# Kernel optimization log

Measured on AMD Instinct MI355X. Metric: run time of the kernel, lower is better.

Reference implementation:

```python
import jax, jax.numpy as jnp
import numpy as np

L = 8          # num_layers
D = 1024       # embed_size
H = 16         # num_heads
M = 4096       # mlp_size
V = 64         # token_size
TMAX = 2048    # max_tokens
B, T = 4, 2048
EPS = 1e-5


def setup_inputs() -> dict:
    key = jax.random.key(0)
    ks = jax.random.split(key, 16)
    s = 0.02
    return {
        "toks": jax.random.normal(ks[0], (B, T, V), dtype=jnp.float32),
        "W_tok": jax.random.normal(ks[1], (D, V), dtype=jnp.float32) * s,    # token_embedding.weight [out,in]
        "W_pos": jax.random.normal(ks[2], (D, TMAX), dtype=jnp.float32) * s,  # postn_embedding.weight
        "Wqkv": jax.random.normal(ks[3], (L, 3 * D, D), dtype=jnp.float32) * s,
        "g1": jnp.ones((L, D), dtype=jnp.float32),
        "be1": jnp.zeros((L, D), dtype=jnp.float32),
        "W1": jax.random.normal(ks[4], (L, M, D), dtype=jnp.float32) * s,
        "bm1": jnp.zeros((L, M), dtype=jnp.float32),
        "W2": jax.random.normal(ks[5], (L, D, M), dtype=jnp.float32) * s,
        "bm2": jnp.zeros((L, D), dtype=jnp.float32),
        "g2": jnp.ones((L, D), dtype=jnp.float32),
        "be2": jnp.zeros((L, D), dtype=jnp.float32),
        "gf": jnp.ones((D,), dtype=jnp.float32),
        "bf": jnp.zeros((D,), dtype=jnp.float32),
        "Wun": jax.random.normal(ks[6], (V, D), dtype=jnp.float32) * s,
        "bun": jnp.zeros((V,), dtype=jnp.float32),
    }


def _layernorm(x, g, b):
    mu = jnp.mean(x, axis=-1, keepdims=True)
    var = jnp.mean(jnp.square(x - mu), axis=-1, keepdims=True)
    return (x - mu) * jax.lax.rsqrt(var + EPS) * g + b


def _attention(x, Wqkv, mask):
    Bx, Tx, Dx = x.shape
    c = Dx // H
    # matches torch: view(B,T,H,3c) then split -> Q/K/V interleaved per head
    qkv = (x @ Wqkv.T).reshape(Bx, Tx, H, 3 * c).transpose(0, 2, 1, 3)  # [B,H,T,3c]
    q, k, v = jnp.split(qkv, 3, axis=-1)
    A = jnp.einsum("bhtc,bhsc->bhts", q, k) / (c ** 0.5)
    A = A + mask  # additive log-mask (0 / -inf), as in the torch code
    p = jax.nn.softmax(A, axis=-1)
    y = jnp.einsum("bhts,bhsc->bhtc", p, v)
    return y.transpose(0, 2, 1, 3).reshape(Bx, Tx, Dx)


def reference(toks, W_tok, W_pos, Wqkv, g1, be1, W1, bm1, W2, bm2, g2, be2, gf, bf, Wun, bun):
    Bx, Tx, _ = toks.shape
    mask = jnp.where(jnp.tril(jnp.ones((Tx, Tx), dtype=bool)), 0.0, -jnp.inf).astype(toks.dtype)
    x = toks @ W_tok.T + W_pos.T[:Tx, :]
    for l in range(L):
        # NOTE: DTransformer adds an EXTRA residual around each block: x = x + block(x)
        h = x
        h = h + _attention(_layernorm(h, g1[l], be1[l]), Wqkv[l], mask)
        z = _layernorm(h, g2[l], be2[l])
        h = h + (jax.nn.relu(z @ W1[l].T + bm1[l]) @ W2[l].T + bm2[l])
        x = x + h
    return _layernorm(x, gf, bf) @ Wun.T + bun
```

## Files before the change

### kernel.cpp

```cpp
#include <hip/hip_runtime.h>
#include <cstdint>
#include <cstddef>

#define L_NUM 8
#define D_DIM 1024
#define H_NUM 16
#define C_DIM 64
#define M_DIM 4096
#define V_DIM 64
#define B_SZ 4
#define T_SZ 2048
#define N_TOK (B_SZ * T_SZ)
#define TMAXP 2048
#define QKV_LD (3 * D_DIM)

typedef __bf16 bf16;
typedef bf16 bf16x4 __attribute__((ext_vector_type(4)));
typedef bf16 bf16x8 __attribute__((ext_vector_type(8)));
typedef float f32x4v __attribute__((ext_vector_type(4)));

__device__ __forceinline__ void async16(const bf16* g, bf16* l) {
    __builtin_amdgcn_global_load_lds(
        (const __attribute__((address_space(1))) void*)g,
        (__attribute__((address_space(3))) void*)l, 16, 0, 0);
}

__global__ __launch_bounds__(256) void convert_kernel(const float* __restrict__ src,
                                                      bf16* __restrict__ dst, int n) {
    int i = (blockIdx.x * 256 + threadIdx.x) * 4;
    if (i >= n) return;
    const float4 v = *(const float4*)(src + i);
    bf16x4 o;
    o[0] = (bf16)v.x; o[1] = (bf16)v.y; o[2] = (bf16)v.z; o[3] = (bf16)v.w;
    *(bf16x4*)(dst + i) = o;
}

__global__ __launch_bounds__(256) void transpose_pos(const float* __restrict__ in,
                                                     float* __restrict__ out) {
    __shared__ float tile[32][33];
    const int t0 = blockIdx.x * 32, d0 = blockIdx.y * 32;
    const int tx = threadIdx.x & 31, ty = threadIdx.x >> 5;
#pragma unroll
    for (int j = 0; j < 32; j += 8)
        tile[ty + j][tx] = in[(size_t)(d0 + ty + j) * TMAXP + t0 + tx];
    __syncthreads();
#pragma unroll
    for (int j = 0; j < 32; j += 8)
        out[(size_t)(t0 + ty + j) * D_DIM + d0 + tx] = tile[tx][ty + j];
}

__global__ __launch_bounds__(256) void ln_kernel(const float* __restrict__ x,
                                                 const float* __restrict__ g,
                                                 const float* __restrict__ b,
                                                 bf16* __restrict__ y) {
    const int n = blockIdx.x, tid = threadIdx.x;
    const float4 v = ((const float4*)(x + (size_t)n * D_DIM))[tid];
    float s = v.x + v.y + v.z + v.w;
    float q = v.x * v.x + v.y * v.y + v.z * v.z + v.w * v.w;
#pragma unroll
    for (int off = 32; off > 0; off >>= 1) {
        s += __shfl_xor(s, off);
        q += __shfl_xor(q, off);
    }
    __shared__ float s1[4], s2[4];
    if ((tid & 63) == 0) { s1[tid >> 6] = s; s2[tid >> 6] = q; }
    __syncthreads();
    s = s1[0] + s1[1] + s1[2] + s1[3];
    q = s2[0] + s2[1] + s2[2] + s2[3];
    const float mu = s * (1.f / D_DIM);
    const float var = q * (1.f / D_DIM) - mu * mu;
    const float rs = rsqrtf(var + 1e-5f);
    const float4 gg = ((const float4*)g)[tid];
    const float4 bb = ((const float4*)b)[tid];
    bf16x4 o;
    o[0] = (bf16)((v.x - mu) * rs * gg.x + bb.x);
    o[1] = (bf16)((v.y - mu) * rs * gg.y + bb.y);
    o[2] = (bf16)((v.z - mu) * rs * gg.z + bb.z);
    o[3] = (bf16)((v.w - mu) * rs * gg.w + bb.w);
    ((bf16x4*)(y + (size_t)n * D_DIM))[tid] = o;
}

template <int MODE>
__global__ __launch_bounds__(256) void gemm_bt(const bf16* __restrict__ A,
                                               const bf16* __restrict__ W,
                                               const float* __restrict__ bias,
                                               const float* add1, const float* add2,
                                               float* outF, bf16* outB, int K, int Nc) {
    __shared__ __align__(16) bf16 As[128][64];
    __shared__ __align__(16) bf16 Bs[128][64];
    const int tid = threadIdx.x;
    const int lane = tid & 63, w = tid >> 6;
    const int wm = w >> 1, wn = w & 1;
    const int l15 = lane & 15, quad = lane >> 4;
    const size_t rowbase = (size_t)blockIdx.y * 128;
    const size_t colbase = (size_t)blockIdx.x * 128;
    f32x4v acc[4][4] = {};
    const int rsub = lane >> 3;
    const int schunk = lane & 7;
    const int gchunk = schunk ^ rsub;
    const bf16* Ag = A + (rowbase + w * 32 + rsub) * (size_t)K + gchunk * 8;
    const bf16* Wg = W + (colbase + w * 32 + rsub) * (size_t)K + gchunk * 8;
    bf16* Asl = &As[w * 32][0];
    bf16* Bsl = &Bs[w * 32][0];
    const int swz = l15 & 7;
    for (int k0 = 0; k0 < K; k0 += 64) {
        __syncthreads();
#pragma unroll
        for (int i = 0; i < 4; ++i) {
            async16(Ag + k0 + (size_t)(i * 8) * K, Asl + i * 512);
            async16(Wg + k0 + (size_t)(i * 8) * K, Bsl + i * 512);
        }
        __syncthreads();
#pragma unroll
        for (int kk = 0; kk < 2; ++kk) {
            const int q = kk * 4 + quad;
            bf16x8 af[4], bv[4];
#pragma unroll
            for (int f = 0; f < 4; ++f) {
                af[f] = *(const bf16x8*)&As[wm * 64 + f * 16 + l15][(q ^ swz) * 8];
                bv[f] = *(const bf16x8*)&Bs[wn * 64 + f * 16 + l15][(q ^ swz) * 8];
            }
#pragma unroll
            for (int fm = 0; fm < 4; ++fm)
#pragma unroll
                for (int fn = 0; fn < 4; ++fn)
                    acc[fm][fn] = __builtin_amdgcn_mfma_f32_16x16x32_bf16(af[fm], bv[fn], acc[fm][fn], 0, 0, 0);
        }
    }
    float bcol[4];
    if (MODE == 1 || MODE == 2) {
#pragma unroll
        for (int fn = 0; fn < 4; ++fn) bcol[fn] = bias[colbase + wn * 64 + fn * 16 + l15];
    }
#pragma unroll
    for (int fm = 0; fm < 4; ++fm) {
#pragma unroll
        for (int r = 0; r < 4; ++r) {
            const size_t row = rowbase + wm * 64 + fm * 16 + quad * 4 + r;
            const size_t base = row * (size_t)Nc + colbase + wn * 64 + l15;
#pragma unroll
            for (int fn = 0; fn < 4; ++fn) {
                float v = acc[fm][fn][r];
                const size_t idx = base + fn * 16;
                if (MODE == 0) {
                    outB[idx] = (bf16)v;
                } else if (MODE == 1) {
                    v += bcol[fn];
                    outB[idx] = (bf16)fmaxf(v, 0.f);
                } else if (MODE == 2) {
                    v += bcol[fn] + add1[idx] + add2[idx];
                    outF[idx] = v;
                } else {
                    const size_t t = row & (T_SZ - 1);
                    const size_t col = colbase + wn * 64 + fn * 16 + l15;
                    v += add1[t * (size_t)Nc + col];
                    outF[idx] = v;
                }
            }
        }
    }
}

template <int MODE>
__global__ __launch_bounds__(512, 2) void gemm256_bt(const bf16* __restrict__ A,
                                                     const bf16* __restrict__ W,
                                                     const float* __restrict__ bias,
                                                     float* outF, bf16* outB, int K, int Nc) {
    __shared__ __align__(16) bf16 As[2][256][64];
    __shared__ __align__(16) bf16 Bs[2][256][64];
    const int tid = threadIdx.x;
    const int lane = tid & 63, w = tid >> 6;
    const int wm = w >> 2, wn = w & 3;
    const int l15 = lane & 15, quad = lane >> 4;
    const size_t rowbase = (size_t)blockIdx.y * 256;
    const size_t colbase = (size_t)blockIdx.x * 256;
    f32x4v acc[8][4] = {};
    const int rsub = lane >> 3;
    const int schunk = lane & 7;
    const int gchunk = schunk ^ rsub;
    const bf16* Ag = A + (rowbase + w * 32 + rsub) * (size_t)K + gchunk * 8;
    const bf16* Wg = W + (colbase + w * 32 + rsub) * (size_t)K + gchunk * 8;
    const int swz = l15 & 7;
    const int nk = K / 64;
#pragma unroll
    for (int i = 0; i < 4; ++i) {
        async16(Ag + (size_t)(i * 8) * K, &As[0][w * 32][0] + i * 512);
        async16(Wg + (size_t)(i * 8) * K, &Bs[0][w * 32][0] + i * 512);
    }
    __syncthreads();
    for (int t = 0; t < nk; ++t) {
        const int cur = t & 1;
        if (t + 1 < nk) {
            const size_t ko = (size_t)(t + 1) * 64;
#pragma unroll
            for (int i = 0; i < 4; ++i) {
                async16(Ag + ko + (size_t)(i * 8) * K, &As[cur ^ 1][w * 32][0] + i * 512);
                async16(Wg + ko + (size_t)(i * 8) * K, &Bs[cur ^ 1][w * 32][0] + i * 512);
            }
        }
        __builtin_amdgcn_s_setprio(1);
#pragma unroll
        for (int kk = 0; kk < 2; ++kk) {
            const int q = kk * 4 + quad;
            bf16x8 af[8], bv[4];
#pragma unroll
            for (int f = 0; f < 8; ++f)
                af[f] = *(const bf16x8*)&As[cur][wm * 128 + f * 16 + l15][(q ^ swz) * 8];
#pragma unroll
            for (int f = 0; f < 4; ++f)
                bv[f] = *(const bf16x8*)&Bs[cur][wn * 64 + f * 16 + l15][(q ^ swz) * 8];
#pragma unroll
            for (int fm = 0; fm < 8; ++fm)
#pragma unroll
                for (int fn = 0; fn < 4; ++fn)
                    acc[fm][fn] = __builtin_amdgcn_mfma_f32_16x16x32_bf16(af[fm], bv[fn], acc[fm][fn], 0, 0, 0);
        }
        __builtin_amdgcn_s_setprio(0);
        __syncthreads();
    }
    float bcol[4];
    if (MODE == 1) {
#pragma unroll
        for (int fn = 0; fn < 4; ++fn) bcol[fn] = bias[colbase + wn * 64 + fn * 16 + l15];
    }
#pragma unroll
    for (int fm = 0; fm < 8; ++fm) {
#pragma unroll
        for (int r = 0; r < 4; ++r) {
            const size_t row = rowbase + wm * 128 + fm * 16 + quad * 4 + r;
            const size_t base = row * (size_t)Nc + colbase + wn * 64 + l15;
#pragma unroll
            for (int fn = 0; fn < 4; ++fn) {
                float v = acc[fm][fn][r];
                const size_t idx = base + fn * 16;
                if (MODE == 1) {
                    v += bcol[fn];
                    outB[idx] = (bf16)fmaxf(v, 0.f);
                } else {
                    outF[idx] = v;
                }
            }
        }
    }
}

__global__ __launch_bounds__(256) void attn_kernel(const bf16* __restrict__ qkv,
                                                   const float* __restrict__ x,
                                                   float* __restrict__ h) {
    constexpr int NQT = T_SZ / 128;
    const int pair = blockIdx.x;
    const int hh = blockIdx.y, b = blockIdx.z;
    const int tid = threadIdx.x;
    const int lane = tid & 63, w = tid >> 6;
    const int quad = lane >> 4, l15 = lane & 15;

    __shared__ __align__(16) bf16 Ks[64][64];
    __shared__ __align__(16) bf16 Vt[64][72];
    __shared__ __align__(16) bf16 Ps[4][16][80];

    constexpr float SC = 0.125f * 1.44269504f;

    const int krow = lane >> 3;
    const int kchunk = lane & 7;
    const int kswz = kchunk ^ krow;
    const bf16* kbase = qkv + ((size_t)(b * T_SZ) + w * 16 + krow) * QKV_LD +
                        hh * 192 + 64 + kchunk * 8;
    const bf16* vbase0 = qkv + ((size_t)(b * T_SZ) + w * 8) * QKV_LD + hh * 192 + 128 + lane;
    const bf16* vbase1 = qkv + ((size_t)(b * T_SZ) + (w + 4) * 8) * QKV_LD + hh * 192 + 128 + lane;

    for (int half = 0; half < 2; ++half) {
        const int qt = half ? (NQT - 1 - pair) : pair;
        const int qwave = qt * 128 + w * 32;
        const int nst = 2 * qt + 2;

        bf16x8 Qf[2][2];
#pragma unroll
        for (int qsub = 0; qsub < 2; ++qsub)
#pragma unroll
            for (int kc = 0; kc < 2; ++kc)
                Qf[qsub][kc] = *(const bf16x8*)(qkv +
                    ((size_t)(b * T_SZ + qt * 128 + w * 32 + qsub * 16 + l15)) * QKV_LD +
                    hh * 192 + kc * 32 + quad * 8);

        f32x4v accO[2][4] = {};
        float m_[2] = {-1e30f, -1e30f}, l_[2] = {0.f, 0.f};

        const bf16* kptr = kbase;
        const bf16* vptr0 = vbase0;
        const bf16* vptr1 = vbase1;

        uint4 kr0 = *(const uint4*)(kptr);
        uint4 kr1 = *(const uint4*)(kptr + (size_t)8 * QKV_LD);
        bf16x8 vv0, vv1;
#pragma unroll
        for (int j = 0; j < 8; ++j) { vv0[j] = vptr0[(size_t)j * QKV_LD]; vv1[j] = vptr1[(size_t)j * QKV_LD]; }
        kptr += (size_t)64 * QKV_LD; vptr0 += (size_t)64 * QKV_LD; vptr1 += (size_t)64 * QKV_LD;

        for (int st = 0; st < nst; ++st) {
            const int sbase = st * 64;
            __syncthreads();
            *(uint4*)&Ks[w * 16 + krow][kswz * 8] = kr0;
            *(uint4*)&Ks[w * 16 + 8 + krow][kswz * 8] = kr1;
            *(bf16x8*)&Vt[lane][w * 8] = vv0;
            *(bf16x8*)&Vt[lane][(w + 4) * 8] = vv1;
            __syncthreads();
            if (st + 1 < nst) {
                kr0 = *(const uint4*)(kptr);
                kr1 = *(const uint4*)(kptr + (size_t)8 * QKV_LD);
#pragma unroll
                for (int j = 0; j < 8; ++j) { vv0[j] = vptr0[(size_t)j * QKV_LD]; vv1[j] = vptr1[(size_t)j * QKV_LD]; }
                kptr += (size_t)64 * QKV_LD; vptr0 += (size_t)64 * QKV_LD; vptr1 += (size_t)64 * QKV_LD;
            }
            if (sbase <= qwave + 31) {
#pragma unroll
                for (int qsub = 0; qsub < 2; ++qsub) {
                    const int qb = qwave + qsub * 16;
                    f32x4v St[4] = {};
                    __builtin_amdgcn_s_setprio(1);
#pragma unroll
                    for (int ssub = 0; ssub < 4; ++ssub)
#pragma unroll
                        for (int kc = 0; kc < 2; ++kc) {
                            bf16x8 Kf = *(const bf16x8*)&Ks[ssub * 16 + l15][((kc * 4 + quad) ^ (l15 & 7)) * 8];
                            St[ssub] = __builtin_amdgcn_mfma_f32_16x16x32_bf16(Kf, Qf[qsub][kc], St[ssub], 0, 0, 0);
                        }
                    __builtin_amdgcn_s_setprio(0);
                    float sv[4][4];
#pragma unroll
                    for (int ssub = 0; ssub < 4; ++ssub)
#pragma unroll
                        for (int r = 0; r < 4; ++r) sv[ssub][r] = St[ssub][r] * SC;
                    if (sbase + 63 > qb) {
#pragma unroll
                        for (int ssub = 0; ssub < 4; ++ssub) {
#pragma unroll
                            for (int r = 0; r < 4; ++r) {
                                const int s = sbase + ssub * 16 + quad * 4 + r;
                                if (s > qb + l15) sv[ssub][r] = -1e38f;
                            }
                        }
                    }
                    float mx = sv[0][0];
#pragma unroll
                    for (int ssub = 0; ssub < 4; ++ssub)
#pragma unroll
                        for (int r = 0; r < 4; ++r) mx = fmaxf(mx, sv[ssub][r]);
                    mx = fmaxf(mx, __shfl_xor(mx, 16));
                    mx = fmaxf(mx, __shfl_xor(mx, 32));
                    const float mold = m_[qsub];
                    const float mnew = fmaxf(mold, mx);
                    const float al = exp2f(mold - mnew);
                    float rs = 0.f;
                    float p[4][4];
#pragma unroll
                    for (int ssub = 0; ssub < 4; ++ssub)
#pragma unroll
                        for (int r = 0; r < 4; ++r) {
                            p[ssub][r] = exp2f(sv[ssub][r] - mnew);
                            rs += p[ssub][r];
                        }
                    rs += __shfl_xor(rs, 16);
                    rs += __shfl_xor(rs, 32);
                    l_[qsub] = l_[qsub] * al + rs;
                    m_[qsub] = mnew;
#pragma unroll
                    for (int ssub = 0; ssub < 4; ++ssub) {
                        bf16x4 pk;
#pragma unroll
                        for (int r = 0; r < 4; ++r) pk[r] = (bf16)p[ssub][r];
                        *(bf16x4*)&Ps[w][l15][ssub * 16 + quad * 4] = pk;
                    }
                    float alr[4];
#pragma unroll
                    for (int r = 0; r < 4; ++r) alr[r] = __shfl(al, quad * 4 + r);
#pragma unroll
                    for (int nsub = 0; nsub < 4; ++nsub)
#pragma unroll
                        for (int r = 0; r < 4; ++r) accO[qsub][nsub][r] *= alr[r];
                    __builtin_amdgcn_s_setprio(1);
#pragma unroll
                    for (int kc2 = 0; kc2 < 2; ++kc2) {
                        bf16x8 Pf = *(const bf16x8*)&Ps[w][l15][kc2 * 32 + quad * 8];
#pragma unroll
                        for (int nsub = 0; nsub < 4; ++nsub) {
                            bf16x8 Vf = *(const bf16x8*)&Vt[nsub * 16 + l15][kc2 * 32 + quad * 8];
                            accO[qsub][nsub] =
                                __builtin_amdgcn_mfma_f32_16x16x32_bf16(Pf, Vf, accO[qsub][nsub], 0, 0, 0);
                        }
                    }
                    __builtin_amdgcn_s_setprio(0);
                }
            }
        }
#pragma unroll
        for (int qsub = 0; qsub < 2; ++qsub) {
            const float linv = 1.f / l_[qsub];
            float invr[4];
#pragma unroll
            for (int r = 0; r < 4; ++r) invr[r] = __shfl(linv, quad * 4 + r);
#pragma unroll
            for (int r = 0; r < 4; ++r) {
                const size_t row = (size_t)(b * T_SZ + qt * 128 + w * 32 + qsub * 16 + quad * 4 + r);
                const size_t base = row * D_DIM + (size_t)hh * 64 + l15;
#pragma unroll
                for (int nsub = 0; nsub < 4; ++nsub) {
                    const size_t idx = base + nsub * 16;
                    h[idx] = x[idx] + accO[qsub][nsub][r] * invr[r];
                }
            }
        }
    }
}

__global__ __launch_bounds__(256) void unembed_kernel(const bf16* __restrict__ A,
                                                      const bf16* __restrict__ W,
                                                      const float* __restrict__ bun,
                                                      float* __restrict__ out) {
    __shared__ __align__(16) bf16 As[128][64];
    __shared__ __align__(16) bf16 Ws[64][64];
    const int tid = threadIdx.x, lane = tid & 63, w = tid >> 6;
    const int l15 = lane & 15, quad = lane >> 4;
    const size_t rowbase = (size_t)blockIdx.x * 128;
    const int rsub = lane >> 3, schunk = lane & 7, gchunk = schunk ^ rsub;
    const bf16* Ag = A + (rowbase + w * 32 + rsub) * (size_t)D_DIM + gchunk * 8;
    const bf16* Wg = W + (w * 16 + rsub) * (size_t)D_DIM + gchunk * 8;
    bf16* Asl = &As[w * 32][0];
    bf16* Wsl = &Ws[w * 16][0];
    const int swz = l15 & 7;
    f32x4v acc[2][4] = {};
    for (int k0 = 0; k0 < D_DIM; k0 += 64) {
        __syncthreads();
#pragma unroll
        for (int i = 0; i < 4; ++i)
            async16(Ag + k0 + (size_t)(i * 8) * D_DIM, Asl + i * 512);
#pragma unroll
        for (int i = 0; i < 2; ++i)
            async16(Wg + k0 + (size_t)(i * 8) * D_DIM, Wsl + i * 512);
        __syncthreads();
#pragma unroll
        for (int kk = 0; kk < 2; ++kk) {
            const int q = kk * 4 + quad;
            bf16x8 af[2], bv[4];
#pragma unroll
            for (int f = 0; f < 2; ++f) af[f] = *(const bf16x8*)&As[w * 32 + f * 16 + l15][(q ^ swz) * 8];
#pragma unroll
            for (int f = 0; f < 4; ++f) bv[f] = *(const bf16x8*)&Ws[f * 16 + l15][(q ^ swz) * 8];
#pragma unroll
            for (int fm = 0; fm < 2; ++fm)
#pragma unroll
                for (int fn = 0; fn < 4; ++fn)
                    acc[fm][fn] = __builtin_amdgcn_mfma_f32_16x16x32_bf16(af[fm], bv[fn], acc[fm][fn], 0, 0, 0);
        }
    }
#pragma unroll
    for (int fm = 0; fm < 2; ++fm)
#pragma unroll
        for (int r = 0; r < 4; ++r) {
            const size_t row = rowbase + w * 32 + fm * 16 + quad * 4 + r;
#pragma unroll
            for (int fn = 0; fn < 4; ++fn) {
                const int col = fn * 16 + l15;
                out[row * V_DIM + col] = acc[fm][fn][r] + bun[col];
            }
        }
}

extern "C" void kernel_launch(void* const* d_in, const int* in_sizes, int n_in,
                              void* d_out, int out_size, void* d_ws, size_t ws_size,
                              hipStream_t stream) {
    (void)in_sizes; (void)n_in; (void)out_size;
    const float* toks = (const float*)d_in[0];
    const float* wtok = (const float*)d_in[1];
    const float* wpos = (const float*)d_in[2];
    const float* wqkv = (const float*)d_in[3];
    const float* g1   = (const float*)d_in[4];
    const float* be1  = (const float*)d_in[5];
    const float* w1   = (const float*)d_in[6];
    const float* bm1  = (const float*)d_in[7];
    const float* w2   = (const float*)d_in[8];
    const float* bm2  = (const float*)d_in[9];
    const float* g2   = (const float*)d_in[10];
    const float* be2  = (const float*)d_in[11];
    const float* gf   = (const float*)d_in[12];
    const float* bfp  = (const float*)d_in[13];
    const float* wun  = (const float*)d_in[14];
    const float* bun  = (const float*)d_in[15];
    float* out = (float*)d_out;

    char* ws = (char*)d_ws;
    size_t off = 0;
    auto take = [&](size_t n) { char* p = ws + off; off += (n + 255) & ~(size_t)255; return p; };
    float* xf   = (float*)take((size_t)N_TOK * D_DIM * 4);
    float* hf   = (float*)take((size_t)N_TOK * D_DIM * 4);
    bf16* lnb   = (bf16*)take((size_t)N_TOK * D_DIM * 2);
    bf16* qkvb  = (bf16*)take((size_t)N_TOK * 3 * D_DIM * 2);
    bf16* a1b   = (bf16*)take((size_t)N_TOK * M_DIM * 2);
    bf16* toksb = (bf16*)take((size_t)N_TOK * V_DIM * 2);
    bf16* wtokb = (bf16*)take((size_t)D_DIM * V_DIM * 2);
    bf16* wunb  = (bf16*)take((size_t)V_DIM * D_DIM * 2);
    float* posT = (float*)take((size_t)TMAXP * D_DIM * 4);

    const size_t perL_q = (size_t)3 * D_DIM * D_DIM;
    const size_t perL_1 = (size_t)M_DIM * D_DIM;
    const size_t perL_2 = (size_t)D_DIM * M_DIM;
    const size_t all_bytes = (size_t)L_NUM * (perL_q + perL_1 + perL_2) * 2 + 4096;
    const bool pre = (ws_size > off) && (ws_size - off >= all_bytes);

    bf16 *wqb, *w1b, *w2b;
    if (pre) {
        wqb = (bf16*)take((size_t)L_NUM * perL_q * 2);
        w1b = (bf16*)take((size_t)L_NUM * perL_1 * 2);
        w2b = (bf16*)take((size_t)L_NUM * perL_2 * 2);
    } else {
        wqb = (bf16*)take(perL_q * 2);
        w1b = (bf16*)take(perL_1 * 2);
        w2b = (bf16*)take(perL_2 * 2);
    }

    convert_kernel<<<(N_TOK * V_DIM) / 1024, 256, 0, stream>>>(toks, toksb, N_TOK * V_DIM);
    convert_kernel<<<(D_DIM * V_DIM) / 1024, 256, 0, stream>>>(wtok, wtokb, D_DIM * V_DIM);
    transpose_pos<<<dim3(TMAXP / 32, D_DIM / 32), 256, 0, stream>>>(wpos, posT);
    gemm_bt<3><<<dim3(D_DIM / 128, N_TOK / 128), 256, 0, stream>>>(
        toksb, wtokb, nullptr, posT, nullptr, xf, nullptr, V_DIM, D_DIM);

    if (pre) {
        convert_kernel<<<(int)((L_NUM * perL_q) / 1024), 256, 0, stream>>>(
            wqkv, wqb, (int)(L_NUM * perL_q));
        convert_kernel<<<(int)((L_NUM * perL_1) / 1024), 256, 0, stream>>>(
            w1, w1b, (int)(L_NUM * perL_1));
        convert_kernel<<<(int)((L_NUM * perL_2) / 1024), 256, 0, stream>>>(
            w2, w2b, (int)(L_NUM * perL_2));
    }

    for (int l = 0; l < L_NUM; ++l) {
        bf16* wq_l = pre ? wqb + (size_t)l * perL_q : wqb;
        bf16* w1_l = pre ? w1b + (size_t)l * perL_1 : w1b;
        bf16* w2_l = pre ? w2b + (size_t)l * perL_2 : w2b;
        if (!pre)
            convert_kernel<<<(int)(perL_q / 1024), 256, 0, stream>>>(
                wqkv + (size_t)l * perL_q, wq_l, (int)perL_q);
        ln_kernel<<<N_TOK, 256, 0, stream>>>(xf, g1 + l * D_DIM, be1 + l * D_DIM, lnb);
        gemm_bt<0><<<dim3(3 * D_DIM / 128, N_TOK / 128), 256, 0, stream>>>(
            lnb, wq_l, nullptr, nullptr, nullptr, nullptr, qkvb, D_DIM, 3 * D_DIM);
        attn_kernel<<<dim3(T_SZ / 256, H_NUM, B_SZ), 256, 0, stream>>>(qkvb, xf, hf);
        ln_kernel<<<N_TOK, 256, 0, stream>>>(hf, g2 + l * D_DIM, be2 + l * D_DIM, lnb);
        if (!pre)
            convert_kernel<<<(int)(perL_1 / 1024), 256, 0, stream>>>(
                w1 + (size_t)l * perL_1, w1_l, (int)perL_1);
        gemm256_bt<1><<<dim3(M_DIM / 256, N_TOK / 256), 512, 0, stream>>>(
            lnb, w1_l, bm1 + l * M_DIM, nullptr, a1b, D_DIM, M_DIM);
        if (!pre)
            convert_kernel<<<(int)(perL_2 / 1024), 256, 0, stream>>>(
                w2 + (size_t)l * perL_2, w2_l, (int)perL_2);
        gemm_bt<2><<<dim3(D_DIM / 128, N_TOK / 128), 256, 0, stream>>>(
            a1b, w2_l, bm2 + l * D_DIM, xf, hf, xf, nullptr, M_DIM, D_DIM);
    }
    ln_kernel<<<N_TOK, 256, 0, stream>>>(xf, gf, bfp, lnb);
    convert_kernel<<<(V_DIM * D_DIM) / 1024, 256, 0, stream>>>(wun, wunb, V_DIM * D_DIM);
    unembed_kernel<<<N_TOK / 128, 256, 0, stream>>>(lnb, wunb, bun, out);
}
```

Measured before the change: 3.582 ms.

## Use 8-wave attention blocks with one query tile per wave, add XCD block swizzle

The attention kernel moves from 4 waves each handling 32 query rows (two 16-row subtiles) to 8 waves each handling 16 rows. Each wave now loads one K row-chunk and one V column-chunk per stage, which spreads the load work and lowers per-wave register use, aiming for more parallelism and latency hiding. The GEMM kernels also remap block indices so consecutive blocks go to the same XCD, intended to improve L2 reuse of shared A/W tiles. In exchange, the attention kernel has more threads per block competing at the barriers, and each K/V stage is amortised over fewer query rows per wave.

Result: faster. 3.360 ms (-6.2%).

```diff
diff --git a/kernel.cpp b/kernel.cpp
--- a/kernel.cpp
+++ b/kernel.cpp
@@ -23,6 +23,15 @@
     __builtin_amdgcn_global_load_lds(
         (const __attribute__((address_space(1))) void*)g,
         (__attribute__((address_space(3))) void*)l, 16, 0, 0);
+}
+
+__device__ __forceinline__ void xcd_swz(int& bx, int& by) {
+    const int gx = (int)gridDim.x;
+    const int nwg = gx * (int)gridDim.y;
+    int lin = (int)blockIdx.y * gx + (int)blockIdx.x;
+    lin = (lin & 7) * (nwg >> 3) + (lin >> 3);
+    by = lin / gx;
+    bx = lin - by * gx;
 }
 
 __global__ __launch_bounds__(256) void convert_kernel(const float* __restrict__ src,
@@ -92,8 +101,10 @@
     const int lane = tid & 63, w = tid >> 6;
     const int wm = w >> 1, wn = w & 1;
     const int l15 = lane & 15, quad = lane >> 4;
-    const size_t rowbase = (size_t)blockIdx.y * 128;
-    const size_t colbase = (size_t)blockIdx.x * 128;
+    int bx, by;
+    xcd_swz(bx, by);
+    const size_t rowbase = (size_t)by * 128;
+    const size_t colbase = (size_t)bx * 128;
     f32x4v acc[4][4] = {};
     const int rsub = lane >> 3;
     const int schunk = lane & 7;
@@ -172,8 +183,10 @@
     const int lane = tid & 63, w = tid >> 6;
     const int wm = w >> 2, wn = w & 3;
     const int l15 = lane & 15, quad = lane >> 4;
-    const size_t rowbase = (size_t)blockIdx.y * 256;
-    const size_t colbase = (size_t)blockIdx.x * 256;
+    int bx, by;
+    xcd_swz(bx, by);
+    const size_t rowbase = (size_t)by * 256;
+    const size_t colbase = (size_t)bx * 256;
     f32x4v acc[8][4] = {};
     const int rsub = lane >> 3;
     const int schunk = lane & 7;
@@ -244,9 +257,9 @@
     }
 }
 
-__global__ __launch_bounds__(256) void attn_kernel(const bf16* __restrict__ qkv,
-                                                   const float* __restrict__ x,
-                                                   float* __restrict__ h) {
+__global__ __launch_bounds__(512, 4) void attn_kernel(const bf16* __restrict__ qkv,
+                                                      const float* __restrict__ x,
+                                                      float* __restrict__ h) {
     constexpr int NQT = T_SZ / 128;
     const int pair = blockIdx.x;
     const int hh = blockIdx.y, b = blockIdx.z;
@@ -256,156 +269,144 @@
 
     __shared__ __align__(16) bf16 Ks[64][64];
     __shared__ __align__(16) bf16 Vt[64][72];
-    __shared__ __align__(16) bf16 Ps[4][16][80];
+    __shared__ __align__(16) bf16 Ps[8][16][80];
 
     constexpr float SC = 0.125f * 1.44269504f;
 
     const int krow = lane >> 3;
     const int kchunk = lane & 7;
     const int kswz = kchunk ^ krow;
-    const bf16* kbase = qkv + ((size_t)(b * T_SZ) + w * 16 + krow) * QKV_LD +
+    const bf16* kbase = qkv + ((size_t)(b * T_SZ) + w * 8 + krow) * QKV_LD +
                         hh * 192 + 64 + kchunk * 8;
-    const bf16* vbase0 = qkv + ((size_t)(b * T_SZ) + w * 8) * QKV_LD + hh * 192 + 128 + lane;
-    const bf16* vbase1 = qkv + ((size_t)(b * T_SZ) + (w + 4) * 8) * QKV_LD + hh * 192 + 128 + lane;
+    const bf16* vbase = qkv + ((size_t)(b * T_SZ) + w * 8) * QKV_LD + hh * 192 + 128 + lane;
 
     for (int half = 0; half < 2; ++half) {
         const int qt = half ? (NQT - 1 - pair) : pair;
-        const int qwave = qt * 128 + w * 32;
+        const int qwave = qt * 128 + w * 16;
         const int nst = 2 * qt + 2;
 
-        bf16x8 Qf[2][2];
-#pragma unroll
-        for (int qsub = 0; qsub < 2; ++qsub)
-#pragma unroll
-            for (int kc = 0; kc < 2; ++kc)
-                Qf[qsub][kc] = *(const bf16x8*)(qkv +
-                    ((size_t)(b * T_SZ + qt * 128 + w * 32 + qsub * 16 + l15)) * QKV_LD +
-                    hh * 192 + kc * 32 + quad * 8);
-
-        f32x4v accO[2][4] = {};
-        float m_[2] = {-1e30f, -1e30f}, l_[2] = {0.f, 0.f};
+        bf16x8 Qf[2];
+#pragma unroll
+        for (int kc = 0; kc < 2; ++kc)
+            Qf[kc] = *(const bf16x8*)(qkv +
+                ((size_t)(b * T_SZ + qwave + l15)) * QKV_LD +
+                hh * 192 + kc * 32 + quad * 8);
+
+        f32x4v accO[4] = {};
+        float m_ = -1e30f, l_ = 0.f;
 
         const bf16* kptr = kbase;
-        const bf16* vptr0 = vbase0;
-        const bf16* vptr1 = vbase1;
+        const bf16* vptr = vbase;
 
         uint4 kr0 = *(const uint4*)(kptr);
-        uint4 kr1 = *(const uint4*)(kptr + (size_t)8 * QKV_LD);
-        bf16x8 vv0, vv1;
-#pragma unroll
-        for (int j = 0; j < 8; ++j) { vv0[j] = vptr0[(size_t)j * QKV_LD]; vv1[j] = vptr1[(size_t)j * QKV_LD]; }
-        kptr += (size_t)64 * QKV_LD; vptr0 += (size_t)64 * QKV_LD; vptr1 += (size_t)64 * QKV_LD;
+        bf16x8 vv0;
+#pragma unroll
+        for (int j = 0; j < 8; ++j) vv0[j] = vptr[(size_t)j * QKV_LD];
+        kptr += (size_t)64 * QKV_LD; vptr += (size_t)64 * QKV_LD;
 
         for (int st = 0; st < nst; ++st) {
             const int sbase = st * 64;
             __syncthreads();
-            *(uint4*)&Ks[w * 16 + krow][kswz * 8] = kr0;
-            *(uint4*)&Ks[w * 16 + 8 + krow][kswz * 8] = kr1;
+            *(uint4*)&Ks[w * 8 + krow][kswz * 8] = kr0;
             *(bf16x8*)&Vt[lane][w * 8] = vv0;
-            *(bf16x8*)&Vt[lane][(w + 4) * 8] = vv1;
             __syncthreads();
             if (st + 1 < nst) {
                 kr0 = *(const uint4*)(kptr);
-                kr1 = *(const uint4*)(kptr + (size_t)8 * QKV_LD);
-#pragma unroll
-                for (int j = 0; j < 8; ++j) { vv0[j] = vptr0[(size_t)j * QKV_LD]; vv1[j] = vptr1[(size_t)j * QKV_LD]; }
-                kptr += (size_t)64 * QKV_LD; vptr0 += (size_t)64 * QKV_LD; vptr1 += (size_t)64 * QKV_LD;
-            }
-            if (sbase <= qwave + 31) {
-#pragma unroll
-                for (int qsub = 0; qsub < 2; ++qsub) {
-                    const int qb = qwave + qsub * 16;
-                    f32x4v St[4] = {};
-                    __builtin_amdgcn_s_setprio(1);
-#pragma unroll
-                    for (int ssub = 0; ssub < 4; ++ssub)
-#pragma unroll
-                        for (int kc = 0; kc < 2; ++kc) {
-                            bf16x8 Kf = *(const bf16x8*)&Ks[ssub * 16 + l15][((kc * 4 + quad) ^ (l15 & 7)) * 8];
-                            St[ssub] = __builtin_amdgcn_mfma_f32_16x16x32_bf16(Kf, Qf[qsub][kc], St[ssub], 0, 0, 0);
-                        }
-                    __builtin_amdgcn_s_setprio(0);
-                    float sv[4][4];
-#pragma unroll
-                    for (int ssub = 0; ssub < 4; ++ssub)
-#pragma unroll
-                        for (int r = 0; r < 4; ++r) sv[ssub][r] = St[ssub][r] * SC;
-                    if (sbase + 63 > qb) {
-#pragma unroll
-                        for (int ssub = 0; ssub < 4; ++ssub) {
-#pragma unroll
-                            for (int r = 0; r < 4; ++r) {
-                                const int s = sbase + ssub * 16 + quad * 4 + r;
-                                if (s > qb + l15) sv[ssub][r] = -1e38f;
-                            }
+#pragma unroll
+                for (int j = 0; j < 8; ++j) vv0[j] = vptr[(size_t)j * QKV_LD];
+                kptr += (size_t)64 * QKV_LD; vptr += (size_t)64 * QKV_LD;
+            }
+            if (sbase <= qwave + 15) {
+                const int qb = qwave;
+                f32x4v St[4] = {};
+                __builtin_amdgcn_s_setprio(1);
+#pragma unroll
+                for (int ssub = 0; ssub < 4; ++ssub)
+#pragma unroll
+                    for (int kc = 0; kc < 2; ++kc) {
+                        bf16x8 Kf = *(const bf16x8*)&Ks[ssub * 16 + l15][((kc * 4 + quad) ^ (l15 & 7)) * 8];
+                        St[ssub] = __builtin_amdgcn_mfma_f32_16x16x32_bf16(Kf, Qf[kc], St[ssub], 0, 0, 0);
+                    }
+                __builtin_amdgcn_s_setprio(0);
+                float sv[4][4];
+#pragma unroll
+                for (int ssub = 0; ssub < 4; ++ssub)
+#pragma unroll
+                    for (int r = 0; r < 4; ++r) sv[ssub][r] = St[ssub][r] * SC;
+                if (sbase + 63 > qb) {
+#pragma unroll
+                    for (int ssub = 0; ssub < 4; ++ssub) {
+#pragma unroll
+                        for (int r = 0; r < 4; ++r) {
+                            const int s = sbase + ssub * 16 + quad * 4 + r;
+                            if (s > qb + l15) sv[ssub][r] = -1e38f;
                         }
                     }
-                    float mx = sv[0][0];
-#pragma unroll
-                    for (int ssub = 0; ssub < 4; ++ssub)
-#pragma unroll
-                        for (int r = 0; r < 4; ++r) mx = fmaxf(mx, sv[ssub][r]);
-                    mx = fmaxf(mx, __shfl_xor(mx, 16));
-                    mx = fmaxf(mx, __shfl_xor(mx, 32));
-                    const float mold = m_[qsub];
-                    const float mnew = fmaxf(mold, mx);
-                    const float al = exp2f(mold - mnew);
-                    float rs = 0.f;
-                    float p[4][4];
-#pragma unroll
-                    for (int ssub = 0; ssub < 4; ++ssub)
-#pragma unroll
-                        for (int r = 0; r < 4; ++r) {
-                            p[ssub][r] = exp2f(sv[ssub][r] - mnew);
-                            rs += p[ssub][r];
-                        }
-                    rs += __shfl_xor(rs, 16);
-                    rs += __shfl_xor(rs, 32);
-                    l_[qsub] = l_[qsub] * al + rs;
-                    m_[qsub] = mnew;
-#pragma unroll
-                    for (int ssub = 0; ssub < 4; ++ssub) {
-                        bf16x4 pk;
-#pragma unroll
-                        for (int r = 0; r < 4; ++r) pk[r] = (bf16)p[ssub][r];
-                        *(bf16x4*)&Ps[w][l15][ssub * 16 + quad * 4] = pk;
+                }
+                float mx = sv[0][0];
+#pragma unroll
+                for (int ssub = 0; ssub < 4; ++ssub)
+#pragma unroll
+                    for (int r = 0; r < 4; ++r) mx = fmaxf(mx, sv[ssub][r]);
+                mx = fmaxf(mx, __shfl_xor(mx, 16));
+                mx = fmaxf(mx, __shfl_xor(mx, 32));
+                const float mold = m_;
+                const float mnew = fmaxf(mold, mx);
+                const float al = exp2f(mold - mnew);
+                float rs = 0.f;
+                float p[4][4];
+#pragma unroll
+                for (int ssub = 0; ssub < 4; ++ssub)
+#pragma unroll
+                    for (int r = 0; r < 4; ++r) {
+                        p[ssub][r] = exp2f(sv[ssub][r] - mnew);
+                        rs += p[ssub][r];
                     }
-                    float alr[4];
-#pragma unroll
-                    for (int r = 0; r < 4; ++r) alr[r] = __shfl(al, quad * 4 + r);
-#pragma unroll
-                    for (int nsub = 0; nsub < 4; ++nsub)
-#pragma unroll
-                        for (int r = 0; r < 4; ++r) accO[qsub][nsub][r] *= alr[r];
-                    __builtin_amdgcn_s_setprio(1);
-#pragma unroll
-                    for (int kc2 = 0; kc2 < 2; ++kc2) {
-                        bf16x8 Pf = *(const bf16x8*)&Ps[w][l15][kc2 * 32 + quad * 8];
-#pragma unroll
-                        for (int nsub = 0; nsub < 4; ++nsub) {
-                            bf16x8 Vf = *(const bf16x8*)&Vt[nsub * 16 + l15][kc2 * 32 + quad * 8];
-                            accO[qsub][nsub] =
-                                __builtin_amdgcn_mfma_f32_16x16x32_bf16(Pf, Vf, accO[qsub][nsub], 0, 0, 0);
-                        }
+                rs += __shfl_xor(rs, 16);
+                rs += __shfl_xor(rs, 32);
+                l_ = l_ * al + rs;
+                m_ = mnew;
+#pragma unroll
+                for (int ssub = 0; ssub < 4; ++ssub) {
+                    bf16x4 pk;
+#pragma unroll
+                    for (int r = 0; r < 4; ++r) pk[r] = (bf16)p[ssub][r];
+                    *(bf16x4*)&Ps[w][l15][ssub * 16 + quad * 4] = pk;
+                }
+                float alr[4];
+#pragma unroll
+                for (int r = 0; r < 4; ++r) alr[r] = __shfl(al, quad * 4 + r);
+#pragma unroll
+                for (int nsub = 0; nsub < 4; ++nsub)
+#pragma unroll
+                    for (int r = 0; r < 4; ++r) accO[nsub][r] *= alr[r];
+                __builtin_amdgcn_s_setprio(1);
+#pragma unroll
+                for (int kc2 = 0; kc2 < 2; ++kc2) {
+                    bf16x8 Pf = *(const bf16x8*)&Ps[w][l15][kc2 * 32 + quad * 8];
+#pragma unroll
+                    for (int nsub = 0; nsub < 4; ++nsub) {
+                        bf16x8 Vf = *(const bf16x8*)&Vt[nsub * 16 + l15][kc2 * 32 + quad * 8];
+                        accO[nsub] =
+                            __builtin_amdgcn_mfma_f32_16x16x32_bf16(Pf, Vf, accO[nsub], 0, 0, 0);
                     }
-                    __builtin_amdgcn_s_setprio(0);
                 }
-            }
-        }
-#pragma unroll
-        for (int qsub = 0; qsub < 2; ++qsub) {
-            const float linv = 1.f / l_[qsub];
+                __builtin_amdgcn_s_setprio(0);
+            }
+        }
+        {
+            const float linv = 1.f / l_;
             float invr[4];
 #pragma unroll
             for (int r = 0; r < 4; ++r) invr[r] = __shfl(linv, quad * 4 + r);
 #pragma unroll
             for (int r = 0; r < 4; ++r) {
-                const size_t row = (size_t)(b * T_SZ + qt * 128 + w * 32 + qsub * 16 + quad * 4 + r);
+                const size_t row = (size_t)(b * T_SZ + qwave + quad * 4 + r);
                 const size_t base = row * D_DIM + (size_t)hh * 64 + l15;
 #pragma unroll
                 for (int nsub = 0; nsub < 4; ++nsub) {
                     const size_t idx = base + nsub * 16;
-                    h[idx] = x[idx] + accO[qsub][nsub][r] * invr[r];
+                    h[idx] = x[idx] + accO[nsub][r] * invr[r];
                 }
             }
         }
@@ -542,7 +543,7 @@
         ln_kernel<<<N_TOK, 256, 0, stream>>>(xf, g1 + l * D_DIM, be1 + l * D_DIM, lnb);
         gemm_bt<0><<<dim3(3 * D_DIM / 128, N_TOK / 128), 256, 0, stream>>>(
             lnb, wq_l, nullptr, nullptr, nullptr, nullptr, qkvb, D_DIM, 3 * D_DIM);
-        attn_kernel<<<dim3(T_SZ / 256, H_NUM, B_SZ), 256, 0, stream>>>(qkvb, xf, hf);
+        attn_kernel<<<dim3(T_SZ / 256, H_NUM, B_SZ), 512, 0, stream>>>(qkvb, xf, hf);
         ln_kernel<<<N_TOK, 256, 0, stream>>>(hf, g2 + l * D_DIM, be2 + l * D_DIM, lnb);
         if (!pre)
             convert_kernel<<<(int)(perL_1 / 1024), 256, 0, stream>>>(
```
